# Performance work log

Measured on AMD Instinct MI355X. Metric: run time of the kernel, lower is better.

## Reference

```python
import jax, jax.numpy as jnp
import numpy as np

H, C, OC, WIN = 12, 768, 768, 4
HD = C // H  # 64
B, T = 4, 1024


def setup_inputs() -> dict:
    key = jax.random.key(0)
    ks = jax.random.split(key, 8)
    s = C ** -0.5  # xavier-ish scale for 1x1 convs
    rel_s = HD ** -0.5
    return {
        "x": jax.random.normal(ks[0], (B, C, T), jnp.float32),
        "c": jax.random.normal(ks[1], (B, C, T), jnp.float32),
        "mask": jnp.ones((B, 1, T, T), jnp.float32),
        "wq": jax.random.normal(ks[2], (C, C), jnp.float32) * s,
        "bq": jnp.zeros((C,), jnp.float32),
        "wk": jax.random.normal(ks[3], (C, C), jnp.float32) * s,
        "bk": jnp.zeros((C,), jnp.float32),
        "wv": jax.random.normal(ks[4], (C, C), jnp.float32) * s,
        "bv": jnp.zeros((C,), jnp.float32),
        "wo": jax.random.normal(ks[5], (OC, C), jnp.float32) * s,
        "bo": jnp.zeros((OC,), jnp.float32),
        "emb_rel_k": jax.random.normal(ks[6], (H, 2 * WIN + 1, HD), jnp.float32) * rel_s,
        "emb_rel_v": jax.random.normal(ks[7], (H, 2 * WIN + 1, HD), jnp.float32) * rel_s,
    }


def _conv1x1(x, w, b):
    # Conv1d(kernel_size=1): pointwise linear over channels. x:(b,c,t) w:(o,c)
    return jnp.einsum('oc,bct->bot', w, x) + b[None, :, None]


def _get_rel_emb(emb, t):
    pad = max(t - WIN, 0)
    start = max(WIN + 1 - t, 0)
    emb = jnp.pad(emb, ((0, 0), (pad, pad), (0, 0)))
    return emb[:, start:start + 2 * t - 1, :]


def _rel_to_abs(x):
    # (b,h,t,2t-1) -> (b,h,t,t) via the pad/reshape skew trick
    b, h, t, _ = x.shape
    x = jnp.pad(x, ((0, 0), (0, 0), (0, 0), (0, 1))).reshape(b, h, 2 * t * t)
    x = jnp.pad(x, ((0, 0), (0, 0), (0, t - 1))).reshape(b, h, t + 1, 2 * t - 1)
    return x[:, :, :t, t - 1:]


def _abs_to_rel(x):
    # (b,h,t,t) -> (b,h,t,2t-1) via inverse skew trick
    b, h, t, _ = x.shape
    x = jnp.pad(x, ((0, 0), (0, 0), (0, 0), (0, t - 1))).reshape(b, h, t * (2 * t - 1))
    x = jnp.pad(x, ((0, 0), (0, 0), (t, 0))).reshape(b, h, t, 2 * t)
    return x[:, :, :, 1:]


def reference(x, c, mask, wq, bq, wk, bk, wv, bv, wo, bo, emb_rel_k, emb_rel_v):
    b, _, t = x.shape
    scale = HD ** -0.5
    # (b,c,t) -> (b,h,t,hd)
    q = _conv1x1(x, wq, bq).reshape(b, H, HD, t).transpose(0, 1, 3, 2)
    k = _conv1x1(c, wk, bk).reshape(b, H, HD, t).transpose(0, 1, 3, 2)
    v = _conv1x1(c, wv, bv).reshape(b, H, HD, t).transpose(0, 1, 3, 2)
    scores = jnp.einsum('bhqd,bhkd->bhqk', q, k) * scale  # (b,h,t,t)
    rel_k = _get_rel_emb(emb_rel_k, t)                    # (h,2t-1,d)
    rel_logits = jnp.einsum('bhtd,hmd->bhtm', q, rel_k)   # (b,h,t,2t-1)
    scores = scores + _rel_to_abs(rel_logits) * scale
    scores = jnp.where(mask == 0, jnp.float32(-1e4), scores)
    attn = jax.nn.softmax(scores, axis=-1)
    out = jnp.einsum('bhqk,bhkd->bhqd', attn, v)
    rel_v = _get_rel_emb(emb_rel_v, t)
    out = out + jnp.einsum('bhtm,hmd->bhtd', _abs_to_rel(attn), rel_v)
    out = out.transpose(0, 1, 3, 2).reshape(b, C, t)      # (b,c,t)
    return _conv1x1(out, wo, bo)
```

## Files before the change

### kernel.cpp

```cpp
#include <hip/hip_runtime.h>
#include <stdint.h>
#include <stddef.h>

#define B_ 4
#define T_ 1024
#define C_ 768
#define H_ 12
#define QSCALE 0.18033688011112042f
#define MASKPEN -14427.0f

typedef __attribute__((ext_vector_type(4))) float f32x4;
typedef __attribute__((ext_vector_type(8))) short s16x8;
typedef __attribute__((ext_vector_type(4))) float float4v;

typedef const __attribute__((address_space(1))) uint32_t ga_u32;
typedef __attribute__((address_space(3))) uint32_t lds_u32;

__device__ __forceinline__ float bf2f(uint16_t u) {
    union { uint32_t u; float f; } cv; cv.u = ((uint32_t)u) << 16; return cv.f;
}
__device__ __forceinline__ uint16_t f2bf(float f) {
    union { float f; uint32_t u; } cv; cv.f = f;
    uint32_t u = cv.u;
    return (uint16_t)((u + 0x7FFFu + ((u >> 16) & 1u)) >> 16);
}
__device__ __forceinline__ void gload16(const uint16_t* g, uint16_t* l) {
    __builtin_amdgcn_global_load_lds((ga_u32*)g, (lds_u32*)l, 16, 0, 0);
}

__global__ void transpose_bf16_kernel(const float* __restrict__ x,
                                      const float* __restrict__ c,
                                      uint16_t* __restrict__ xT,
                                      uint16_t* __restrict__ cT) {
    __shared__ float tile[32][33];
    const int which = blockIdx.z;
    const int b = blockIdx.y;
    const int t0 = (blockIdx.x % (T_ / 32)) * 32;
    const int c0 = (blockIdx.x / (T_ / 32)) * 32;
    const float* src = (which ? c : x) + (size_t)b * C_ * T_;
    uint16_t* dst = (which ? cT : xT) + (size_t)b * T_ * C_;
    const int lj = threadIdx.x & 31, li = threadIdx.x >> 5;
    #pragma unroll
    for (int i = li; i < 32; i += 8)
        tile[i][lj] = src[(size_t)(c0 + i) * T_ + t0 + lj];
    __syncthreads();
    #pragma unroll
    for (int i = li; i < 32; i += 8)
        dst[(size_t)(t0 + i) * C_ + c0 + lj] = f2bf(tile[lj][i]);
}

__global__ void convert_weights_kernel(const float* __restrict__ wq,
                                       const float* __restrict__ wk,
                                       const float* __restrict__ wv,
                                       const float* __restrict__ wo,
                                       uint16_t* __restrict__ out) {
    const int which = blockIdx.y;
    const float* w = (which == 0) ? wq : (which == 1) ? wk : (which == 2) ? wv : wo;
    const float sc = (which == 0) ? QSCALE : 1.0f;
    uint16_t* dst = out + (size_t)which * C_ * C_;
    const int i = (blockIdx.x * 256 + threadIdx.x) * 4;
    float4v v = *(const float4v*)(w + i);
    uint32_t lo = (uint32_t)f2bf(v[0] * sc) | ((uint32_t)f2bf(v[1] * sc) << 16);
    uint32_t hi = (uint32_t)f2bf(v[2] * sc) | ((uint32_t)f2bf(v[3] * sc) << 16);
    uint32_t* d32 = (uint32_t*)(dst + i);
    d32[0] = lo; d32[1] = hi;
}

__global__ void mask_bits_kernel(const float* __restrict__ mask,
                                 uint32_t* __restrict__ bits) {
    const size_t i = (size_t)blockIdx.x * 256 + threadIdx.x;
    const float m = mask[i];
    unsigned long long bal = __ballot(m != 0.0f);
    const int lane = threadIdx.x & 63;
    if (lane == 0)       bits[i >> 5] = (uint32_t)bal;
    else if (lane == 32) bits[i >> 5] = (uint32_t)(bal >> 32);
}

template <bool OPROJ>
__global__ __launch_bounds__(256, 2)
void gemm_kernel(const uint16_t* __restrict__ xT, const uint16_t* __restrict__ cT,
                 const uint16_t* __restrict__ wb,
                 const float* __restrict__ bq, const float* __restrict__ bk,
                 const float* __restrict__ bv, const float* __restrict__ bo,
                 const uint16_t* __restrict__ attT,
                 uint16_t* __restrict__ Qb, uint16_t* __restrict__ Kb,
                 uint16_t* __restrict__ Vb, float* __restrict__ outp) {
    const int tid = threadIdx.x;
    const int z = blockIdx.z;

    const uint16_t* A; const uint16_t* Bm; const float* bias;
    uint16_t* Cb = nullptr; float* Cf = nullptr;
    int N, ldc; bool bias_col; float bscale = 1.0f;
    if (!OPROJ) {
        const int bat = z & 3, which = z >> 2;
        if (which == 0) {
            A = xT + (size_t)bat * T_ * C_; Bm = wb;                bias = bq;
            Cb = Qb + (size_t)bat * T_ * C_; N = C_; ldc = C_; bias_col = true;
            bscale = QSCALE;
        } else if (which == 1) {
            A = cT + (size_t)bat * T_ * C_; Bm = wb + 1 * C_ * C_;  bias = bk;
            Cb = Kb + (size_t)bat * T_ * C_; N = C_; ldc = C_; bias_col = true;
        } else {
            A = wb + 2 * (size_t)C_ * C_;   Bm = cT + (size_t)(z & 3) * T_ * C_; bias = bv;
            Cb = Vb + (size_t)bat * C_ * T_; N = T_; ldc = T_; bias_col = false;
        }
    } else {
        A = wb + 3 * (size_t)C_ * C_; Bm = attT + (size_t)z * T_ * C_; bias = bo;
        Cf = outp + (size_t)z * C_ * T_; N = T_; ldc = T_; bias_col = false;
    }
    const int tn_cnt = N / 128;
    const int tm = blockIdx.x / tn_cnt, tn = blockIdx.x % tn_cnt;
    const int row0 = tm * 128, col0 = tn * 128;

    __shared__ uint16_t As[128 * 64];
    __shared__ uint16_t Bs[128 * 64];

    const int w = tid >> 6, l = tid & 63;
    const int wr = w & 1, wc = w >> 1;

    const f32x4 zz = {0.f, 0.f, 0.f, 0.f};
    f32x4 acc[4][4];
    #pragma unroll
    for (int i = 0; i < 4; ++i)
        #pragma unroll
        for (int j = 0; j < 4; ++j) acc[i][j] = zz;

    const int sr = tid >> 3, sp = tid & 7;

    for (int kt = 0; kt < 12; ++kt) {
        const int k0 = kt * 64;
        #pragma unroll
        for (int it = 0; it < 4; ++it) {
            const int row = it * 32 + sr;
            const int cch = sp ^ (row & 7);
            gload16(A + (size_t)(row0 + row) * 768 + k0 + cch * 8, &As[row * 64 + sp * 8]);
        }
        #pragma unroll
        for (int it = 0; it < 4; ++it) {
            const int row = it * 32 + sr;
            const int cch = sp ^ (row & 7);
            gload16(Bm + (size_t)(col0 + row) * 768 + k0 + cch * 8, &Bs[row * 64 + sp * 8]);
        }
        __syncthreads();

        #pragma unroll
        for (int kk = 0; kk < 2; ++kk) {
            s16x8 af[4], bf[4];
            #pragma unroll
            for (int i = 0; i < 4; ++i) {
                const int arow = wr * 64 + i * 16 + (l & 15);
                const int ach = (kk * 4 + (l >> 4)) ^ (arow & 7);
                af[i] = *(const s16x8*)(&As[arow * 64 + ach * 8]);
                const int brow = wc * 64 + i * 16 + (l & 15);
                const int bch = (kk * 4 + (l >> 4)) ^ (brow & 7);
                bf[i] = *(const s16x8*)(&Bs[brow * 64 + bch * 8]);
            }
            #pragma unroll
            for (int i = 0; i < 4; ++i)
                #pragma unroll
                for (int j = 0; j < 4; ++j)
                    acc[i][j] = __builtin_amdgcn_mfma_f32_16x16x32_bf16(af[i], bf[j], acc[i][j], 0, 0, 0);
        }
        __syncthreads();
    }

    #pragma unroll
    for (int i = 0; i < 4; ++i) {
        const int rowb = row0 + wr * 64 + i * 16 + ((l >> 4) * 4);
        #pragma unroll
        for (int j = 0; j < 4; ++j) {
            const int col = col0 + wc * 64 + j * 16 + (l & 15);
            const float bc = bias_col ? bias[col] * bscale : 0.f;
            #pragma unroll
            for (int r = 0; r < 4; ++r) {
                const int row = rowb + r;
                const float v = acc[i][j][r] + (bias_col ? bc : bias[row]);
                if (!OPROJ) Cb[(size_t)row * ldc + col] = f2bf(v);
                else        Cf[(size_t)row * ldc + col] = v;
            }
        }
    }
}

__global__ __launch_bounds__(256, 2)
void attn_kernel(const uint16_t* __restrict__ Qb, const uint16_t* __restrict__ Kb,
                 const uint16_t* __restrict__ Vb, const uint32_t* __restrict__ mbits,
                 const float* __restrict__ emb_k, const float* __restrict__ emb_v,
                 uint16_t* __restrict__ attT) {
    const int i0 = blockIdx.x * 64;
    const int h = blockIdx.y, b = blockIdx.z;
    const int tid = threadIdx.x, w = tid >> 6, l = tid & 63;

    __shared__ uint16_t Ks[2][64 * 64];
    __shared__ uint16_t Vs[2][64 * 64];
    __shared__ uint16_t Ps[64 * 72];
    __shared__ float rk[64 * 9];
    __shared__ float sband[64 * 9];
    __shared__ int s_allones;

    const uint16_t* Kbase = Kb + (size_t)b * T_ * C_ + h * 64;
    const uint16_t* Vbase = Vb + (size_t)b * C_ * T_ + (size_t)(h * 64) * T_;
    const uint32_t* mrow = mbits + (size_t)b * T_ * 32;
    const int sr = tid >> 3, sp = tid & 7;

    auto stage = [&](int jt, int buf) {
        const int j0s = jt * 64;
        #pragma unroll
        for (int it = 0; it < 2; ++it) {
            const int row = it * 32 + sr;
            const int cch = sp ^ (row & 7);
            gload16(Kbase + (size_t)(j0s + row) * C_ + cch * 8, &Ks[buf][row * 64 + sp * 8]);
        }
        #pragma unroll
        for (int it = 0; it < 2; ++it) {
            const int row = it * 32 + sr;
            const int cch = sp ^ (row & 7);
            gload16(Vbase + (size_t)row * T_ + j0s + cch * 8, &Vs[buf][row * 64 + sp * 8]);
        }
    };

    stage(0, 0);

    bool mok = true;
    {
        const uint32_t* mb = mrow + (size_t)i0 * 32;
        #pragma unroll
        for (int it = 0; it < 8; ++it) mok &= (mb[it * 256 + tid] == 0xFFFFFFFFu);
    }

    s16x8 qf[2];
    {
        const int row = i0 + w * 16 + (l & 15);
        const uint16_t* qp = Qb + ((size_t)(b * T_ + row)) * C_ + h * 64 + (l >> 4) * 8;
        qf[0] = *(const s16x8*)(qp);
        qf[1] = *(const s16x8*)(qp + 32);
    }
    for (int t = tid; t < 64 * 9; t += 256) {
        const int rr = t % 9, row = t / 9;
        const uint32_t* q32 = (const uint32_t*)(Qb + ((size_t)(b * T_ + i0 + row)) * C_ + h * 64);
        const float* ep = emb_k + ((size_t)h * 9 + rr) * 64;
        float s = 0.f;
        #pragma unroll
        for (int d2 = 0; d2 < 32; ++d2) {
            const uint32_t u = q32[d2];
            s += bf2f((uint16_t)u) * ep[2 * d2] + bf2f((uint16_t)(u >> 16)) * ep[2 * d2 + 1];
        }
        rk[t] = s;
        sband[t] = -1e30f;
    }
    if (tid == 0) s_allones = 1;
    __syncthreads();
    if (!mok) s_allones = 0;
    __syncthreads();
    const bool maskones = (s_allones != 0);

    float m[4], lsum[4];
    const f32x4 zz = {0.f, 0.f, 0.f, 0.f};
    f32x4 oacc[4] = {zz, zz, zz, zz};
    #pragma unroll
    for (int r = 0; r < 4; ++r) { m[r] = -1e30f; lsum[r] = 0.f; }

    const int iMin = i0 + w * 16, iMax = iMin + 15;

    for (int jt = 0; jt < 16; ++jt) {
        const int cur = jt & 1;
        if (jt < 15) stage(jt + 1, cur ^ 1);
        const int j0 = jt * 64;

        float sv[4][4];
        #pragma unroll
        for (int tn = 0; tn < 4; ++tn) {
            f32x4 s = zz;
            #pragma unroll
            for (int kk = 0; kk < 2; ++kk) {
                const int krow = tn * 16 + (l & 15);
                const int kch = (kk * 4 + (l >> 4)) ^ (krow & 7);
                s16x8 kf = *(const s16x8*)(&Ks[cur][krow * 64 + kch * 8]);
                s = __builtin_amdgcn_mfma_f32_16x16x32_bf16(qf[kk], kf, s, 0, 0, 0);
            }
            #pragma unroll
            for (int r = 0; r < 4; ++r) sv[tn][r] = s[r];
        }

        const bool bandTile = (j0 <= iMax + 5) && (j0 + 63 >= iMin - 3);
        if (bandTile) {
            #pragma unroll
            for (int tn = 0; tn < 4; ++tn)
                #pragma unroll
                for (int r = 0; r < 4; ++r) {
                    const int iloc = w * 16 + (l >> 4) * 4 + r;
                    const int rr = (j0 + tn * 16 + (l & 15)) - (i0 + iloc) + 3;
                    if ((unsigned)rr < 9u) sv[tn][r] += rk[iloc * 9 + rr];
                }
        }
        if (!maskones) {
            #pragma unroll
            for (int r = 0; r < 4; ++r) {
                const int i = i0 + w * 16 + (l >> 4) * 4 + r;
                const uint32_t m0 = mrow[(size_t)i * 32 + (j0 >> 5)];
                const uint32_t m1 = mrow[(size_t)i * 32 + (j0 >> 5) + 1];
                #pragma unroll
                for (int tn = 0; tn < 4; ++tn) {
                    const uint32_t mw = (tn < 2) ? m0 : m1;
                    const int bit = (tn * 16 + (l & 15)) & 31;
                    if (!((mw >> bit) & 1u)) sv[tn][r] = MASKPEN;
                }
            }
        }
        if (bandTile) {
            #pragma unroll
            for (int tn = 0; tn < 4; ++tn)
                #pragma unroll
                for (int r = 0; r < 4; ++r) {
                    const int iloc = w * 16 + (l >> 4) * 4 + r;
                    const int rr = (j0 + tn * 16 + (l & 15)) - (i0 + iloc) + 3;
                    if ((unsigned)rr < 9u) sband[iloc * 9 + rr] = sv[tn][r];
                }
        }

        float rm[4];
        #pragma unroll
        for (int r = 0; r < 4; ++r) {
            float v = fmaxf(fmaxf(sv[0][r], sv[1][r]), fmaxf(sv[2][r], sv[3][r]));
            v = fmaxf(v, __shfl_xor(v, 1));
            v = fmaxf(v, __shfl_xor(v, 2));
            v = fmaxf(v, __shfl_xor(v, 4));
            v = fmaxf(v, __shfl_xor(v, 8));
            rm[r] = v;
        }
        const bool need = (rm[0] > m[0]) | (rm[1] > m[1]) | (rm[2] > m[2]) | (rm[3] > m[3]);
        if (__any(need)) {
            #pragma unroll
            for (int r = 0; r < 4; ++r) {
                const float mn = fmaxf(m[r], rm[r]);
                const float alpha = exp2f(m[r] - mn);
                m[r] = mn;
                lsum[r] *= alpha;
                #pragma unroll
                for (int td = 0; td < 4; ++td) oacc[td][r] *= alpha;
            }
        }
        #pragma unroll
        for (int r = 0; r < 4; ++r) {
            float rs = 0.f;
            #pragma unroll
            for (int tn = 0; tn < 4; ++tn) {
                const float p = exp2f(sv[tn][r] - m[r]);
                sv[tn][r] = p;
                rs += p;
            }
            rs += __shfl_xor(rs, 1);
            rs += __shfl_xor(rs, 2);
            rs += __shfl_xor(rs, 4);
            rs += __shfl_xor(rs, 8);
            lsum[r] += rs;
        }

        #pragma unroll
        for (int tn = 0; tn < 4; ++tn)
            #pragma unroll
            for (int r = 0; r < 4; ++r) {
                const int prow = w * 16 + (l >> 4) * 4 + r;
                Ps[prow * 72 + tn * 16 + (l & 15)] = f2bf(sv[tn][r]);
            }

        #pragma unroll
        for (int ks = 0; ks < 2; ++ks) {
            const int prow = w * 16 + (l & 15);
            s16x8 pf = *(const s16x8*)(&Ps[prow * 72 + ks * 32 + (l >> 4) * 8]);
            #pragma unroll
            for (int td = 0; td < 4; ++td) {
                const int vrow = td * 16 + (l & 15);
                const int vch = (ks * 4 + (l >> 4)) ^ (vrow & 7);
                s16x8 vf = *(const s16x8*)(&Vs[cur][vrow * 64 + vch * 8]);
                oacc[td] = __builtin_amdgcn_mfma_f32_16x16x32_bf16(pf, vf, oacc[td], 0, 0, 0);
            }
        }
        __syncthreads();
    }

    float invl[4];
    #pragma unroll
    for (int r = 0; r < 4; ++r) invl[r] = 1.f / lsum[r];
    float ab[4][9];
    #pragma unroll
    for (int r = 0; r < 4; ++r) {
        const int iloc = w * 16 + (l >> 4) * 4 + r;
        #pragma unroll
        for (int rr = 0; rr < 9; ++rr)
            ab[r][rr] = exp2f(sband[iloc * 9 + rr] - m[r]) * invl[r];
    }
    #pragma unroll
    for (int td = 0; td < 4; ++td) {
        const int d = td * 16 + (l & 15);
        const float* ev = emb_v + (size_t)h * 9 * 64 + d;
        #pragma unroll
        for (int r = 0; r < 4; ++r) {
            float v = oacc[td][r] * invl[r];
            #pragma unroll
            for (int rr = 0; rr < 9; ++rr) v += ab[r][rr] * ev[rr * 64];
            const int i = i0 + w * 16 + (l >> 4) * 4 + r;
            attT[((size_t)(b * T_ + i)) * C_ + h * 64 + d] = f2bf(v);
        }
    }
}

extern "C" void kernel_launch(void* const* d_in, const int* in_sizes, int n_in,
                              void* d_out, int out_size, void* d_ws, size_t ws_size,
                              hipStream_t stream) {
    const float* x    = (const float*)d_in[0];
    const float* c    = (const float*)d_in[1];
    const float* mask = (const float*)d_in[2];
    const float* wq   = (const float*)d_in[3];
    const float* bq   = (const float*)d_in[4];
    const float* wk   = (const float*)d_in[5];
    const float* bk   = (const float*)d_in[6];
    const float* wv   = (const float*)d_in[7];
    const float* bv   = (const float*)d_in[8];
    const float* wo   = (const float*)d_in[9];
    const float* bo   = (const float*)d_in[10];
    const float* ek   = (const float*)d_in[11];
    const float* ev   = (const float*)d_in[12];
    float* out = (float*)d_out;

    uint8_t* ws = (uint8_t*)d_ws;
    size_t off = 0;
    auto alloc = [&](size_t bytes) {
        uint8_t* p = ws + off;
        off += (bytes + 255) & ~(size_t)255;
        return p;
    };
    uint16_t* xT   = (uint16_t*)alloc((size_t)B_ * T_ * C_ * 2);
    uint16_t* cT   = (uint16_t*)alloc((size_t)B_ * T_ * C_ * 2);
    uint16_t* wb   = (uint16_t*)alloc((size_t)4 * C_ * C_ * 2);
    uint16_t* Qb   = (uint16_t*)alloc((size_t)B_ * T_ * C_ * 2);
    uint16_t* Kb   = (uint16_t*)alloc((size_t)B_ * T_ * C_ * 2);
    uint16_t* Vb   = (uint16_t*)alloc((size_t)B_ * C_ * T_ * 2);
    uint16_t* attT = (uint16_t*)alloc((size_t)B_ * T_ * C_ * 2);
    uint32_t* mbits = (uint32_t*)alloc((size_t)B_ * T_ * 32 * 4);

    transpose_bf16_kernel<<<dim3(768, B_, 2), 256, 0, stream>>>(x, c, xT, cT);
    convert_weights_kernel<<<dim3(576, 4), 256, 0, stream>>>(wq, wk, wv, wo, wb);
    mask_bits_kernel<<<dim3((B_ * T_ * T_) / 256), 256, 0, stream>>>(mask, mbits);
    gemm_kernel<false><<<dim3(48, 1, 12), 256, 0, stream>>>(xT, cT, wb, bq, bk, bv, bo,
                                                            attT, Qb, Kb, Vb, out);
    attn_kernel<<<dim3(T_ / 64, H_, B_), 256, 0, stream>>>(Qb, Kb, Vb, mbits, ek, ev, attT);
    gemm_kernel<true><<<dim3(48, 1, 4), 256, 0, stream>>>(xT, cT, wb, bq, bk, bv, bo,
                                                          attT, Qb, Kb, Vb, out);
}
```

Baseline: 254.1 us.

## Use MFMA for rel-k logits, precompute mask flags, defer softmax reductions

Precomputes per-block all-ones mask flags in a separate small kernel and converts emb_rel_k to bf16, so the attention kernel computes rel-k logits with MFMA instead of a scalar per-thread dot loop. It also defers the cross-lane row-max shuffle until a rescale is needed, keeps per-lane partial row sums and reduces them once at the end, and truncates P to bf16 instead of rounding. This cuts prologue latency and per-tile shuffle work in the attention loop, at the cost of two extra small launches and slightly lower precision for P and the rel-k embeddings.

```diff
diff --git a/kernel.cpp b/kernel.cpp
--- a/kernel.cpp
+++ b/kernel.cpp
@@ -23,6 +23,10 @@
     union { float f; uint32_t u; } cv; cv.f = f;
     uint32_t u = cv.u;
     return (uint16_t)((u + 0x7FFFu + ((u >> 16) & 1u)) >> 16);
+}
+__device__ __forceinline__ uint16_t f2bf_trunc(float f) {
+    union { float f; uint32_t u; } cv; cv.f = f;
+    return (uint16_t)(cv.u >> 16);
 }
 __device__ __forceinline__ void gload16(const uint16_t* g, uint16_t* l) {
     __builtin_amdgcn_global_load_lds((ga_u32*)g, (lds_u32*)l, 16, 0, 0);
@@ -66,6 +70,12 @@
     d32[0] = lo; d32[1] = hi;
 }
 
+__global__ void convert_ek_kernel(const float* __restrict__ ek,
+                                  uint16_t* __restrict__ ekb) {
+    const int i = blockIdx.x * 256 + threadIdx.x;
+    ekb[i] = f2bf(ek[i]);
+}
+
 __global__ void mask_bits_kernel(const float* __restrict__ mask,
                                  uint32_t* __restrict__ bits) {
     const size_t i = (size_t)blockIdx.x * 256 + threadIdx.x;
@@ -74,6 +84,21 @@
     const int lane = threadIdx.x & 63;
     if (lane == 0)       bits[i >> 5] = (uint32_t)bal;
     else if (lane == 32) bits[i >> 5] = (uint32_t)(bal >> 32);
+}
+
+__global__ void mask_flags_kernel(const uint32_t* __restrict__ bits,
+                                  uint32_t* __restrict__ flags) {
+    const int b = blockIdx.y, i0 = blockIdx.x * 64;
+    const uint32_t* p = bits + ((size_t)b * T_ + i0) * 32;
+    bool ok = true;
+    #pragma unroll
+    for (int it = 0; it < 8; ++it) ok &= (p[it * 256 + threadIdx.x] == 0xFFFFFFFFu);
+    __shared__ int s_ok[4];
+    const bool wall = __all(ok);
+    if ((threadIdx.x & 63) == 0) s_ok[threadIdx.x >> 6] = wall ? 1 : 0;
+    __syncthreads();
+    if (threadIdx.x == 0)
+        flags[b * 16 + blockIdx.x] = (uint32_t)(s_ok[0] & s_ok[1] & s_ok[2] & s_ok[3]);
 }
 
 template <bool OPROJ>
@@ -185,7 +210,8 @@
 __global__ __launch_bounds__(256, 2)
 void attn_kernel(const uint16_t* __restrict__ Qb, const uint16_t* __restrict__ Kb,
                  const uint16_t* __restrict__ Vb, const uint32_t* __restrict__ mbits,
-                 const float* __restrict__ emb_k, const float* __restrict__ emb_v,
+                 const uint32_t* __restrict__ flags,
+                 const uint16_t* __restrict__ ekb, const float* __restrict__ emb_v,
                  uint16_t* __restrict__ attT) {
     const int i0 = blockIdx.x * 64;
     const int h = blockIdx.y, b = blockIdx.z;
@@ -194,13 +220,12 @@
     __shared__ uint16_t Ks[2][64 * 64];
     __shared__ uint16_t Vs[2][64 * 64];
     __shared__ uint16_t Ps[64 * 72];
+    __shared__ uint16_t Es[16 * 72];
     __shared__ float rk[64 * 9];
     __shared__ float sband[64 * 9];
-    __shared__ int s_allones;
 
     const uint16_t* Kbase = Kb + (size_t)b * T_ * C_ + h * 64;
     const uint16_t* Vbase = Vb + (size_t)b * C_ * T_ + (size_t)(h * 64) * T_;
-    const uint32_t* mrow = mbits + (size_t)b * T_ * 32;
     const int sr = tid >> 3, sp = tid & 7;
 
     auto stage = [&](int jt, int buf) {
@@ -220,13 +245,6 @@
     };
 
     stage(0, 0);
-
-    bool mok = true;
-    {
-        const uint32_t* mb = mrow + (size_t)i0 * 32;
-        #pragma unroll
-        for (int it = 0; it < 8; ++it) mok &= (mb[it * 256 + tid] == 0xFFFFFFFFu);
-    }
 
     s16x8 qf[2];
     {
@@ -235,24 +253,33 @@
         qf[0] = *(const s16x8*)(qp);
         qf[1] = *(const s16x8*)(qp + 32);
     }
-    for (int t = tid; t < 64 * 9; t += 256) {
-        const int rr = t % 9, row = t / 9;
-        const uint32_t* q32 = (const uint32_t*)(Qb + ((size_t)(b * T_ + i0 + row)) * C_ + h * 64);
-        const float* ep = emb_k + ((size_t)h * 9 + rr) * 64;
-        float s = 0.f;
-        #pragma unroll
-        for (int d2 = 0; d2 < 32; ++d2) {
-            const uint32_t u = q32[d2];
-            s += bf2f((uint16_t)u) * ep[2 * d2] + bf2f((uint16_t)(u >> 16)) * ep[2 * d2 + 1];
-        }
-        rk[t] = s;
-        sband[t] = -1e30f;
-    }
-    if (tid == 0) s_allones = 1;
+
+    {
+        const int idx = tid * 4;
+        const int row = idx >> 6, col = idx & 63;
+        uint64_t val = 0;
+        if (row < 9) val = *(const uint64_t*)(ekb + ((size_t)h * 9 + row) * 64 + col);
+        *(uint64_t*)&Es[row * 72 + col] = val;
+    }
+    for (int t = tid; t < 64 * 9; t += 256) sband[t] = -1e30f;
     __syncthreads();
-    if (!mok) s_allones = 0;
-    __syncthreads();
-    const bool maskones = (s_allones != 0);
+
+    {
+        f32x4 racc = {0.f, 0.f, 0.f, 0.f};
+        #pragma unroll
+        for (int kk = 0; kk < 2; ++kk) {
+            s16x8 ef = *(const s16x8*)(&Es[(l & 15) * 72 + (l >> 4) * 8 + kk * 32]);
+            racc = __builtin_amdgcn_mfma_f32_16x16x32_bf16(qf[kk], ef, racc, 0, 0, 0);
+        }
+        if ((l & 15) < 9) {
+            #pragma unroll
+            for (int r = 0; r < 4; ++r)
+                rk[(w * 16 + (l >> 4) * 4 + r) * 9 + (l & 15)] = racc[r];
+        }
+    }
+
+    const bool maskones = (flags[b * 16 + blockIdx.x] != 0);
+    const uint32_t* mrow = mbits + (size_t)b * T_ * 32;
 
     float m[4], lsum[4];
     const f32x4 zz = {0.f, 0.f, 0.f, 0.f};
@@ -318,21 +345,20 @@
                 }
         }
 
-        float rm[4];
-        #pragma unroll
-        for (int r = 0; r < 4; ++r) {
-            float v = fmaxf(fmaxf(sv[0][r], sv[1][r]), fmaxf(sv[2][r], sv[3][r]));
-            v = fmaxf(v, __shfl_xor(v, 1));
-            v = fmaxf(v, __shfl_xor(v, 2));
-            v = fmaxf(v, __shfl_xor(v, 4));
-            v = fmaxf(v, __shfl_xor(v, 8));
-            rm[r] = v;
-        }
-        const bool need = (rm[0] > m[0]) | (rm[1] > m[1]) | (rm[2] > m[2]) | (rm[3] > m[3]);
+        float mx[4];
+        #pragma unroll
+        for (int r = 0; r < 4; ++r)
+            mx[r] = fmaxf(fmaxf(sv[0][r], sv[1][r]), fmaxf(sv[2][r], sv[3][r]));
+        const bool need = (mx[0] > m[0]) | (mx[1] > m[1]) | (mx[2] > m[2]) | (mx[3] > m[3]);
         if (__any(need)) {
             #pragma unroll
             for (int r = 0; r < 4; ++r) {
-                const float mn = fmaxf(m[r], rm[r]);
+                float v = mx[r];
+                v = fmaxf(v, __shfl_xor(v, 1));
+                v = fmaxf(v, __shfl_xor(v, 2));
+                v = fmaxf(v, __shfl_xor(v, 4));
+                v = fmaxf(v, __shfl_xor(v, 8));
+                const float mn = fmaxf(m[r], v);
                 const float alpha = exp2f(m[r] - mn);
                 m[r] = mn;
                 lsum[r] *= alpha;
@@ -342,18 +368,12 @@
         }
         #pragma unroll
         for (int r = 0; r < 4; ++r) {
-            float rs = 0.f;
             #pragma unroll
             for (int tn = 0; tn < 4; ++tn) {
                 const float p = exp2f(sv[tn][r] - m[r]);
                 sv[tn][r] = p;
-                rs += p;
-            }
-            rs += __shfl_xor(rs, 1);
-            rs += __shfl_xor(rs, 2);
-            rs += __shfl_xor(rs, 4);
-            rs += __shfl_xor(rs, 8);
-            lsum[r] += rs;
+                lsum[r] += p;
+            }
         }
 
         #pragma unroll
@@ -361,7 +381,7 @@
             #pragma unroll
             for (int r = 0; r < 4; ++r) {
                 const int prow = w * 16 + (l >> 4) * 4 + r;
-                Ps[prow * 72 + tn * 16 + (l & 15)] = f2bf(sv[tn][r]);
+                Ps[prow * 72 + tn * 16 + (l & 15)] = f2bf_trunc(sv[tn][r]);
             }
 
         #pragma unroll
@@ -381,7 +401,14 @@
 
     float invl[4];
     #pragma unroll
-    for (int r = 0; r < 4; ++r) invl[r] = 1.f / lsum[r];
+    for (int r = 0; r < 4; ++r) {
+        float s = lsum[r];
+        s += __shfl_xor(s, 1);
+        s += __shfl_xor(s, 2);
+        s += __shfl_xor(s, 4);
+        s += __shfl_xor(s, 8);
+        invl[r] = 1.f / s;
+    }
     float ab[4][9];
     #pragma unroll
     for (int r = 0; r < 4; ++r) {
@@ -438,13 +465,18 @@
     uint16_t* Vb   = (uint16_t*)alloc((size_t)B_ * C_ * T_ * 2);
     uint16_t* attT = (uint16_t*)alloc((size_t)B_ * T_ * C_ * 2);
     uint32_t* mbits = (uint32_t*)alloc((size_t)B_ * T_ * 32 * 4);
+    uint16_t* ekb  = (uint16_t*)alloc((size_t)H_ * 9 * 64 * 2);
+    uint32_t* mflags = (uint32_t*)alloc((size_t)B_ * 16 * 4);
 
     transpose_bf16_kernel<<<dim3(768, B_, 2), 256, 0, stream>>>(x, c, xT, cT);
     convert_weights_kernel<<<dim3(576, 4), 256, 0, stream>>>(wq, wk, wv, wo, wb);
+    convert_ek_kernel<<<dim3(27), 256, 0, stream>>>(ek, ekb);
     mask_bits_kernel<<<dim3((B_ * T_ * T_) / 256), 256, 0, stream>>>(mask, mbits);
+    mask_flags_kernel<<<dim3(16, B_), 256, 0, stream>>>(mbits, mflags);
     gemm_kernel<false><<<dim3(48, 1, 12), 256, 0, stream>>>(xT, cT, wb, bq, bk, bv, bo,
                                                             attT, Qb, Kb, Vb, out);
-    attn_kernel<<<dim3(T_ / 64, H_, B_), 256, 0, stream>>>(Qb, Kb, Vb, mbits, ek, ev, attT);
+    attn_kernel<<<dim3(T_ / 64, H_, B_), 256, 0, stream>>>(Qb, Kb, Vb, mbits, mflags,
+                                                           ekb, ev, attT);
     gemm_kernel<true><<<dim3(48, 1, 4), 256, 0, stream>>>(xT, cT, wb, bq, bk, bv, bo,
                                                           attT, Qb, Kb, Vb, out);
 }
```

Result: faster. 220.9 us (-13.0%).
